# Kernel tuning notes

Measured on AMD Instinct MI355X. Metric: run time of the kernel, lower is better.

## Reference

```python
import jax, jax.numpy as jnp
import numpy as np

GS = 128      # quantization group size along K (in_features)
EPS = 1e-8

def setup_inputs() -> dict:
    key = jax.random.key(0)
    k1, k2, k3, k4 = jax.random.split(key, 4)
    B, S, K, N = 4, 2048, 4096, 4096
    x = jax.random.normal(k1, (B, S, K), dtype=jnp.float32)
    weight = jax.random.normal(k2, (N, K), dtype=jnp.float32) * 0.02   # torch Linear layout [out, in]
    bias = jax.random.normal(k3, (N,), dtype=jnp.float32) * 0.01
    # per-group (K//gs) x per-out-channel quant steps, strictly positive
    step_scales = jax.random.uniform(k4, (K // GS, N), dtype=jnp.float32, minval=0.01, maxval=0.05)
    return {"x": x, "weight": weight, "bias": bias, "step_scales": step_scales}

def reference(x, weight, bias, step_scales):
    # w: [K, N] (forward transposes the Linear weight)
    w = weight.T
    K, N = w.shape
    G = K // GS
    wg = w.reshape(G, GS, N)                       # group along K
    s = step_scales[:, None, :] + EPS              # [G, 1, N]
    # group-quantized dequant: round-to-step per (group, out-channel)
    q = jnp.round(wg / s)
    w_dq = (q * s).reshape(K, N)
    out = jnp.einsum('bsk,kn->bsn', x, w_dq)
    if bias is not None:
        out = out + bias
    return out
```

## Files before the change

kernel.cpp:

```cpp
#include <hip/hip_runtime.h>
#include <hip/hip_bf16.h>
#include <stdint.h>

typedef unsigned short u16;
typedef __bf16 bf16x8 __attribute__((ext_vector_type(8)));
typedef float f32x4 __attribute__((ext_vector_type(4)));
typedef unsigned short u16x8 __attribute__((ext_vector_type(8)));

#define QEPS 1e-8f

__device__ __forceinline__ u16 f32_to_bf16_rne(float f) {
    uint32_t u = __float_as_uint(f);
    u += 0x7fffu + ((u >> 16) & 1u);
    return (u16)(u >> 16);
}

__global__ void cvt_x_bf16(const float* __restrict__ x, u16* __restrict__ xb, int n8) {
    int idx = blockIdx.x * blockDim.x + threadIdx.x;
    if (idx >= n8) return;
    const float4* p = (const float4*)(x + (size_t)idx * 8);
    float4 a = p[0], b = p[1];
    u16x8 r;
    r[0] = f32_to_bf16_rne(a.x); r[1] = f32_to_bf16_rne(a.y);
    r[2] = f32_to_bf16_rne(a.z); r[3] = f32_to_bf16_rne(a.w);
    r[4] = f32_to_bf16_rne(b.x); r[5] = f32_to_bf16_rne(b.y);
    r[6] = f32_to_bf16_rne(b.z); r[7] = f32_to_bf16_rne(b.w);
    *(u16x8*)(xb + (size_t)idx * 8) = r;
}

__global__ void dequant_w_bf16(const float* __restrict__ w, const float* __restrict__ ss,
                               u16* __restrict__ wb, int N, int K) {
    int idx = blockIdx.x * blockDim.x + threadIdx.x;
    int pr = K >> 3;
    if (idx >= N * pr) return;
    int n = idx / pr;
    int k8 = (idx - n * pr) << 3;
    float s = ss[(size_t)(k8 >> 7) * N + n] + QEPS;
    const float4* p = (const float4*)(w + (size_t)n * K + k8);
    float4 a = p[0], b = p[1];
    float v[8] = {a.x, a.y, a.z, a.w, b.x, b.y, b.z, b.w};
    u16x8 r;
#pragma unroll
    for (int i = 0; i < 8; ++i) {
        float q = rintf(v[i] / s);
        r[i] = f32_to_bf16_rne(q * s);
    }
    *(u16x8*)(wb + (size_t)n * K + k8) = r;
}

#define BM 256
#define BN 256
#define SLOTB 32768
#define ABYT 16384
#define LDSB 131072

#define ASYNC16(g, l)                                                                      \
    __builtin_amdgcn_global_load_lds((const __attribute__((address_space(1))) void*)(g),   \
                                     (__attribute__((address_space(3))) void*)(l), 16, 0, 0)
#define VMCNT(n) asm volatile("s_waitcnt vmcnt(" #n ")" ::: "memory")
#define BAR()    __builtin_amdgcn_s_barrier()
#define MFMA(a, b, c) __builtin_amdgcn_mfma_f32_16x16x32_bf16((a), (b), (c), 0, 0, 0)

__global__ __launch_bounds__(512, 2) void gemm_bf16_bt_256(
        const u16* __restrict__ A,
        const u16* __restrict__ B,
        const float* __restrict__ bias,
        float* __restrict__ C,
        int M, int N, int K) {
    extern __shared__ char lds[];
    const int tid  = threadIdx.x;
    const int wave = tid >> 6;
    const int lane = tid & 63;

    const int nwg = gridDim.x;
    const int cpx = nwg >> 3;
    const int bid = blockIdx.x;
    const int swz = (bid & 7) * cpx + (bid >> 3);
    const int nbn = N / BN;
    const int bm  = swz / nbn;
    const int bn  = swz - bm * nbn;

    const int wr = wave >> 2;
    const int wc = wave & 3;

    const int srow  = tid >> 2;
    const int kbsrc = ((tid & 3) << 4) ^ (((tid >> 3) & 3) << 4);
    const char* gA0 = (const char*)A + ((size_t)(bm * BM + srow) * K) * 2 + kbsrc;
    const char* gA1 = (const char*)A + ((size_t)(bm * BM + 128 + srow) * K) * 2 + kbsrc;
    const char* gB0 = (const char*)B + ((size_t)(bn * BN + srow) * K) * 2 + kbsrc;
    const char* gB1 = (const char*)B + ((size_t)(bn * BN + 128 + srow) * K) * 2 + kbsrc;

    auto STG = [&](int t, int part) {
        const size_t ko = (size_t)t << 6;
        char* d = lds + ((t & 3) * SLOTB) + (wave << 10);
        if (part == 0)      ASYNC16(gA0 + ko, d);
        else if (part == 1) ASYNC16(gA1 + ko, d + 8192);
        else if (part == 2) ASYNC16(gB0 + ko, d + ABYT);
        else                ASYNC16(gB1 + ko, d + ABYT + 8192);
    };

    const int kx = ((lane >> 4) ^ ((lane >> 1) & 3)) << 4;
    const char* pa = lds + (size_t)(wr * 128 + (lane & 15)) * 64 + kx;
    const char* pb = lds + ABYT + (size_t)(wc * 64 + (lane & 15)) * 64 + kx;

    f32x4 acc[8][4] = {};
    bf16x8 aX[8], bX[4], aY[8], bY[4];

#define RD_B(DST, i) DST[i] = *(const bf16x8*)(pb + bon + (i) * 1024)
#define RD_A(DST, i) DST[i] = *(const bf16x8*)(pa + bon + (i) * 1024)
#define MROW(CA, CB, m)                                                       \
    acc[m][0] = MFMA(CA[m], CB[0], acc[m][0]);                                \
    acc[m][1] = MFMA(CA[m], CB[1], acc[m][1]);                                \
    acc[m][2] = MFMA(CA[m], CB[2], acc[m][2]);                                \
    acc[m][3] = MFMA(CA[m], CB[3], acc[m][3]);

#define SLAB(CA, CB, NA, NB, t, DO_STAGE, DO_NEXT, VMSTMT)                    \
    {                                                                         \
        const int bon = (((t) + 1) & 3) * SLOTB;                              \
        __builtin_amdgcn_s_setprio(1);                                        \
        MROW(CA, CB, 0)                                                       \
        if (DO_NEXT) { RD_B(NB, 0); RD_B(NB, 1); }                            \
        if (DO_STAGE) STG((t) + 3, 0);                                        \
        MROW(CA, CB, 1)                                                       \
        if (DO_NEXT) { RD_B(NB, 2); RD_B(NB, 3); }                            \
        if (DO_STAGE) STG((t) + 3, 1);                                        \
        MROW(CA, CB, 2)                                                       \
        if (DO_NEXT) { RD_A(NA, 0); RD_A(NA, 1); }                            \
        if (DO_STAGE) STG((t) + 3, 2);                                        \
        MROW(CA, CB, 3)                                                       \
        if (DO_NEXT) { RD_A(NA, 2); RD_A(NA, 3); }                            \
        if (DO_STAGE) STG((t) + 3, 3);                                        \
        MROW(CA, CB, 4)                                                       \
        if (DO_NEXT) { RD_A(NA, 4); RD_A(NA, 5); }                            \
        MROW(CA, CB, 5)                                                       \
        if (DO_NEXT) { RD_A(NA, 6); RD_A(NA, 7); }                            \
        MROW(CA, CB, 6)                                                       \
        MROW(CA, CB, 7)                                                       \
        __builtin_amdgcn_s_setprio(0);                                        \
        VMSTMT;                                                               \
        BAR();                                                                \
    }

    const int NT = K >> 5;

    STG(0, 0); STG(0, 1); STG(0, 2); STG(0, 3);
    STG(1, 0); STG(1, 1); STG(1, 2); STG(1, 3);
    STG(2, 0); STG(2, 1); STG(2, 2); STG(2, 3);
    VMCNT(4);
    BAR();
    {
        const int bon = 0;
#pragma unroll
        for (int n = 0; n < 4; ++n) RD_B(bX, n);
#pragma unroll
        for (int m = 0; m < 8; ++m) RD_A(aX, m);
    }

    for (int t = 0; t < NT - 4; t += 2) {
        SLAB(aX, bX, aY, bY, t,     true, true, VMCNT(4))
        SLAB(aY, bY, aX, bX, t + 1, true, true, VMCNT(4))
    }
    SLAB(aX, bX, aY, bY, NT - 4, true,  true,  VMCNT(4))
    SLAB(aY, bY, aX, bX, NT - 3, false, true,  VMCNT(0))
    SLAB(aX, bX, aY, bY, NT - 2, false, true,  (void)0)
    SLAB(aY, bY, aX, bX, NT - 1, false, false, (void)0)

    const int r0 = bm * BM + wr * 128 + ((lane >> 4) << 2);
    const int c0 = bn * BN + wc * 64 + (lane & 15);
    float bv[4];
#pragma unroll
    for (int n = 0; n < 4; ++n) bv[n] = bias[c0 + n * 16];
#pragma unroll
    for (int m = 0; m < 8; ++m)
#pragma unroll
        for (int n = 0; n < 4; ++n)
#pragma unroll
            for (int i = 0; i < 4; ++i)
                C[(size_t)(r0 + m * 16 + i) * N + (c0 + n * 16)] = acc[m][n][i] + bv[n];
}

extern "C" void kernel_launch(void* const* d_in, const int* in_sizes, int n_in,
                              void* d_out, int out_size, void* d_ws, size_t ws_size,
                              hipStream_t stream) {
    const float* x    = (const float*)d_in[0];
    const float* w    = (const float*)d_in[1];
    const float* bias = (const float*)d_in[2];
    const float* ss   = (const float*)d_in[3];
    float* out        = (float*)d_out;

    const int N = in_sizes[2];
    const int K = in_sizes[1] / N;
    const int M = in_sizes[0] / K;

    u16* xb = (u16*)d_ws;
    u16* wb = xb + (size_t)M * K;

    int n8x = (M * K) >> 3;
    cvt_x_bf16<<<(n8x + 255) / 256, 256, 0, stream>>>(x, xb, n8x);

    int n8w = (N * K) >> 3;
    dequant_w_bf16<<<(n8w + 255) / 256, 256, 0, stream>>>(w, ss, wb, N, K);

    (void)hipFuncSetAttribute((const void*)gemm_bf16_bt_256,
                              hipFuncAttributeMaxDynamicSharedMemorySize, LDSB);
    dim3 grid((M / BM) * (N / BN));
    gemm_bf16_bt_256<<<grid, 512, LDSB, stream>>>(xb, wb, bias, out, M, N, K);
}
```

Measured before the change: 266.5 us.

## Use five LDS slots and barrier once per pair of k-tiles

Grows the LDS ring from four to five 32KB slots and tracks slot offsets in rotating registers instead of deriving them from the tile index. Each loop step now computes two k-tiles and then does a single full vmcnt(0) wait plus one barrier, instead of a partial wait and a barrier after every tile. The aim is to halve barrier and synchronisation overhead in the main loop. In exchange, every pair waits for all outstanding async loads, which may expose more global-load latency, and LDS use rises to 160KB per block.

Result: slower. 288.2 us (+8.2%).

```diff
diff --git a/kernel.cpp b/kernel.cpp
--- a/kernel.cpp
+++ b/kernel.cpp
@@ -52,7 +52,7 @@
 #define BN 256
 #define SLOTB 32768
 #define ABYT 16384
-#define LDSB 131072
+#define LDSB 163840
 
 #define ASYNC16(g, l)                                                                      \
     __builtin_amdgcn_global_load_lds((const __attribute__((address_space(1))) void*)(g),   \
@@ -90,9 +90,9 @@
     const char* gB0 = (const char*)B + ((size_t)(bn * BN + srow) * K) * 2 + kbsrc;
     const char* gB1 = (const char*)B + ((size_t)(bn * BN + 128 + srow) * K) * 2 + kbsrc;
 
-    auto STG = [&](int t, int part) {
-        const size_t ko = (size_t)t << 6;
-        char* d = lds + ((t & 3) * SLOTB) + (wave << 10);
+    auto STG = [&](int tS, int boS, int part) {
+        const size_t ko = (size_t)tS << 6;
+        char* d = lds + boS + (wave << 10);
         if (part == 0)      ASYNC16(gA0 + ko, d);
         else if (part == 1) ASYNC16(gA1 + ko, d + 8192);
         else if (part == 2) ASYNC16(gB0 + ko, d + ABYT);
@@ -114,39 +114,48 @@
     acc[m][2] = MFMA(CA[m], CB[2], acc[m][2]);                                \
     acc[m][3] = MFMA(CA[m], CB[3], acc[m][3]);
 
-#define SLAB(CA, CB, NA, NB, t, DO_STAGE, DO_NEXT, VMSTMT)                    \
+#define SLAB_BODY(CA, CB, NA, NB, BON, tS, boS, DO_STG, DO_WV)                \
     {                                                                         \
-        const int bon = (((t) + 1) & 3) * SLOTB;                              \
+        const int bon = (BON);                                                \
         __builtin_amdgcn_s_setprio(1);                                        \
         MROW(CA, CB, 0)                                                       \
-        if (DO_NEXT) { RD_B(NB, 0); RD_B(NB, 1); }                            \
-        if (DO_STAGE) STG((t) + 3, 0);                                        \
+        if (DO_WV) { RD_B(NB, 0); RD_B(NB, 1); }                              \
+        if (DO_STG) STG(tS, boS, 0);                                          \
         MROW(CA, CB, 1)                                                       \
-        if (DO_NEXT) { RD_B(NB, 2); RD_B(NB, 3); }                            \
-        if (DO_STAGE) STG((t) + 3, 1);                                        \
+        if (DO_WV) { RD_B(NB, 2); RD_B(NB, 3); }                              \
+        if (DO_STG) STG(tS, boS, 1);                                          \
         MROW(CA, CB, 2)                                                       \
-        if (DO_NEXT) { RD_A(NA, 0); RD_A(NA, 1); }                            \
-        if (DO_STAGE) STG((t) + 3, 2);                                        \
+        if (DO_WV) { RD_A(NA, 0); RD_A(NA, 1); }                              \
+        if (DO_STG) STG(tS, boS, 2);                                          \
         MROW(CA, CB, 3)                                                       \
-        if (DO_NEXT) { RD_A(NA, 2); RD_A(NA, 3); }                            \
-        if (DO_STAGE) STG((t) + 3, 3);                                        \
+        if (DO_WV) { RD_A(NA, 2); RD_A(NA, 3); }                              \
+        if (DO_STG) STG(tS, boS, 3);                                          \
         MROW(CA, CB, 4)                                                       \
-        if (DO_NEXT) { RD_A(NA, 4); RD_A(NA, 5); }                            \
+        if (DO_WV) { RD_A(NA, 4); RD_A(NA, 5); }                              \
         MROW(CA, CB, 5)                                                       \
-        if (DO_NEXT) { RD_A(NA, 6); RD_A(NA, 7); }                            \
+        if (DO_WV) { RD_A(NA, 6); RD_A(NA, 7); }                              \
         MROW(CA, CB, 6)                                                       \
         MROW(CA, CB, 7)                                                       \
         __builtin_amdgcn_s_setprio(0);                                        \
-        VMSTMT;                                                               \
-        BAR();                                                                \
-    }
+    }
+
+#define PAIR(t, DO_SA, DO_SB, DO_WB)                                          \
+    SLAB_BODY(aX, bX, aY, bY, o1, (t) + 3, o3, DO_SA, true)                   \
+    SLAB_BODY(aY, bY, aX, bX, o2, (t) + 4, o4, DO_SB, DO_WB)                  \
+    VMCNT(0);                                                                 \
+    BAR();
+
+#define ROTATE2() { int r0 = o0, r1 = o1; o0 = o2; o1 = o3; o2 = o4; o3 = r0; o4 = r1; }
 
     const int NT = K >> 5;
 
-    STG(0, 0); STG(0, 1); STG(0, 2); STG(0, 3);
-    STG(1, 0); STG(1, 1); STG(1, 2); STG(1, 3);
-    STG(2, 0); STG(2, 1); STG(2, 2); STG(2, 3);
-    VMCNT(4);
+#pragma unroll
+    for (int p = 0; p < 4; ++p) STG(0, 0, p);
+#pragma unroll
+    for (int p = 0; p < 4; ++p) STG(1, SLOTB, p);
+#pragma unroll
+    for (int p = 0; p < 4; ++p) STG(2, 2 * SLOTB, p);
+    VMCNT(0);
     BAR();
     {
         const int bon = 0;
@@ -156,14 +165,15 @@
         for (int m = 0; m < 8; ++m) RD_A(aX, m);
     }
 
+    int o0 = 0, o1 = SLOTB, o2 = 2 * SLOTB, o3 = 3 * SLOTB, o4 = 4 * SLOTB;
+
     for (int t = 0; t < NT - 4; t += 2) {
-        SLAB(aX, bX, aY, bY, t,     true, true, VMCNT(4))
-        SLAB(aY, bY, aX, bX, t + 1, true, true, VMCNT(4))
-    }
-    SLAB(aX, bX, aY, bY, NT - 4, true,  true,  VMCNT(4))
-    SLAB(aY, bY, aX, bX, NT - 3, false, true,  VMCNT(0))
-    SLAB(aX, bX, aY, bY, NT - 2, false, true,  (void)0)
-    SLAB(aY, bY, aX, bX, NT - 1, false, false, (void)0)
+        PAIR(t, true, true, true)
+        ROTATE2();
+    }
+    PAIR(NT - 4, true, false, true)
+    ROTATE2();
+    PAIR(NT - 2, false, false, false)
 
     const int r0 = bm * BM + wr * 128 + ((lane >> 4) << 2);
     const int c0 = bn * BN + wc * 64 + (lane & 15);
@@ -176,7 +186,7 @@
         for (int n = 0; n < 4; ++n)
 #pragma unroll
             for (int i = 0; i < 4; ++i)
-                C[(size_t)(r0 + m * 16 + i) * N + (c0 + n * 16)] = acc[m][n][i] + bv[n];
+                C[(size_t)(r0 + (m << 4) + i) * N + (c0 + (n << 4))] = acc[m][n][i] + bv[n];
 }
 
 extern "C" void kernel_launch(void* const* d_in, const int* in_sizes, int n_in,
```
